# Kernel optimization log

Hardware: AMD Instinct MI355X
Metric: run time of the kernel (lower is better)

Reference implementation:

```python
import jax, jax.numpy as jnp
import numpy as np

N, E, D = 50000, 800000, 128
CLAMP = 2.0  # coord_weights_clamp_value


def setup_inputs() -> dict:
    key = jax.random.key(0)
    ks = jax.random.split(key, 12)
    rn = lambda k, shape, scale: jax.random.normal(k, shape, jnp.float32) * scale
    s = lambda fan_in: 1.0 / np.sqrt(fan_in)
    h = rn(ks[0], (N, D), 1.0)
    x = rn(ks[1], (N, 3), 1.0)
    edges = jax.random.randint(ks[2], (2, E), 0, N)
    # edge MLP: Linear(2D+1 -> D), SiLU, Linear(D -> D), SiLU
    we1 = rn(ks[3], (2 * D + 1, D), s(2 * D + 1)); be1 = jnp.zeros((D,), jnp.float32)
    we2 = rn(ks[4], (D, D), s(D));                 be2 = jnp.zeros((D,), jnp.float32)
    # node MLP: Linear(2D -> D), SiLU, Linear(D -> D)
    wn1 = rn(ks[5], (2 * D, D), s(2 * D));         bn1 = jnp.zeros((D,), jnp.float32)
    wn2 = rn(ks[6], (D, D), s(D));                 bn2 = jnp.zeros((D,), jnp.float32)
    # coord MLP: Linear(D -> D), SiLU, Linear(D -> 1, no bias, small init)
    wc1 = rn(ks[7], (D, D), s(D));                 bc1 = jnp.zeros((D,), jnp.float32)
    wc2 = rn(ks[8], (D, 1), 0.001)
    return dict(h=h, x=x, edges=edges, we1=we1, be1=be1, we2=we2, be2=be2,
                wn1=wn1, bn1=bn1, wn2=wn2, bn2=bn2, wc1=wc1, bc1=bc1, wc2=wc2)


def reference(h, x, edges, we1, be1, we2, be2, wn1, bn1, wn2, bn2, wc1, bc1, wc2):
    n = h.shape[0]
    row, col = edges[0], edges[1]
    # coord2radial
    coord_diff = x[row] - x[col]                                  # [E, 3]
    radial = jnp.sum(coord_diff * coord_diff, axis=1, keepdims=True)  # [E, 1]
    # edge model: phi_e(h_i, h_j, ||x_i - x_j||^2)
    e_in = jnp.concatenate([h[row], h[col], radial], axis=1)      # [E, 2D+1]
    m = jax.nn.silu(jax.nn.silu(e_in @ we1 + be1) @ we2 + be2)    # [E, D]
    # coord model: x_i += mean_j (x_i - x_j) * phi_x(m_ij), clamped
    w = jax.nn.silu(m @ wc1 + bc1) @ wc2                          # [E, 1]
    trans = jnp.clip(coord_diff * w, -CLAMP, CLAMP)               # [E, 3]
    ones = jnp.ones((row.shape[0], 1), m.dtype)
    cnt = jax.ops.segment_sum(ones, row, num_segments=n)          # [N, 1]
    agg_x = jax.ops.segment_sum(trans, row, num_segments=n) / jnp.maximum(cnt, 1.0)
    x_out = x + agg_x
    # node model: h_i += phi_h(h_i, sum_j m_ij)  (residual=True)
    agg_m = jax.ops.segment_sum(m, row, num_segments=n)           # [N, D]
    h_up = jax.nn.silu(jnp.concatenate([h, agg_m], axis=1) @ wn1 + bn1) @ wn2 + bn2
    h_out = h + h_up
    return (h_out, x_out)
```

## Files before the change

### kernel.cpp

```cpp
#include <hip/hip_runtime.h>
#include <hip/hip_bf16.h>
#include <stdint.h>

typedef unsigned short u16;
typedef __bf16 bf16x8 __attribute__((ext_vector_type(8)));
typedef float f32x4 __attribute__((ext_vector_type(4)));

#define DD 128

__device__ __forceinline__ u16 f2bf(float f) {
  uint32_t r;
  asm("v_cvt_pk_bf16_f32 %0, %1, %2" : "=v"(r) : "v"(f), "v"(f));
  return (u16)r;
}
__device__ __forceinline__ float bf2f(u16 h) {
  union { uint32_t u; float f; } v; v.u = ((uint32_t)h) << 16;
  return v.f;
}
__device__ __forceinline__ uint32_t pack2(float a, float b) {
  uint32_t r;
  asm("v_cvt_pk_bf16_f32 %0, %1, %2" : "=v"(r) : "v"(a), "v"(b));
  return r;
}
__device__ __forceinline__ float silu_(float v) {
  return v * __builtin_amdgcn_rcpf(1.0f + __expf(-v));
}
__device__ __forceinline__ f32x4 MFMA(bf16x8 a, bf16x8 b, f32x4 c) {
  return __builtin_amdgcn_mfma_f32_16x16x32_bf16(a, b, c, 0, 0, 0);
}
#define LGKM_FENCE() do { asm volatile("s_waitcnt lgkmcnt(0)" ::: "memory"); __builtin_amdgcn_sched_barrier(0); } while (0)

__global__ __launch_bounds__(256) void kprep(
    const float* __restrict__ we1, const float* __restrict__ we2,
    const float* __restrict__ wn1, const float* __restrict__ wn2,
    const float* __restrict__ wc1, u16* __restrict__ frags) {
  const int total = 16384 * 5 + 32768;
  for (int idx = blockIdx.x * blockDim.x + threadIdx.x; idx < total;
       idx += gridDim.x * blockDim.x) {
    const float* src; int segbase;
    if (idx < 16384)      { src = we1;          segbase = 0; }
    else if (idx < 32768) { src = we1 + 16384;  segbase = 16384; }
    else if (idx < 49152) { src = we2;          segbase = 32768; }
    else if (idx < 65536) { src = wc1;          segbase = 49152; }
    else if (idx < 81920) { src = wn2;          segbase = 65536; }
    else                  { src = wn1;          segbase = 81920; }
    int local = idx - segbase;
    int k = local >> 7, n = local & 127;
    float v = src[k * 128 + n];
    int s = k >> 5, i = k & 7, g = (k >> 3) & 3;
    int lane = (g << 4) | (n & 15), f = n >> 4;
    frags[segbase + (((s * 8 + f) * 64 + lane) << 3) + i] = f2bf(v);
  }
}

__global__ __launch_bounds__(256) void kpq(
    const float* __restrict__ h, const float* __restrict__ be1,
    const u16* __restrict__ wA, const u16* __restrict__ wB,
    u16* __restrict__ Pb, u16* __restrict__ Qb, int N) {
  __shared__ u16 act[64 * 128];
  const int tid = threadIdx.x;
  const int w = tid >> 6, l = tid & 63;
  const int lm = l & 15, lh = l >> 4;
  const int base = blockIdx.x * 64;

  {
    const int q = l & 3;
    const int rowL = w * 16 + (l >> 2);
    int node = base + rowL; if (node >= N) node = N - 1;
    const float* hs = h + (size_t)node * 128 + q * 32;
    #pragma unroll
    for (int c4 = 0; c4 < 4; ++c4) {
      float4 v0 = *(const float4*)(hs + c4 * 8);
      float4 v1 = *(const float4*)(hs + c4 * 8 + 4);
      uint4 pk;
      pk.x = pack2(v0.x, v0.y); pk.y = pack2(v0.z, v0.w);
      pk.z = pack2(v1.x, v1.y); pk.w = pack2(v1.z, v1.w);
      int c = q * 4 + c4;
      *(uint4*)&act[rowL * 128 + (((c ^ (rowL & 7))) << 3)] = pk;
    }
  }
  LGKM_FENCE();
  const int rowA = w * 16 + lm, sw = rowA & 7;
  bf16x8 a[4];
  #pragma unroll
  for (int s = 0; s < 4; ++s)
    a[s] = *(const bf16x8*)&act[rowA * 128 + (((4 * s + lh) ^ sw) << 3)];
  float be1r[8];
  #pragma unroll
  for (int f = 0; f < 8; ++f) be1r[f] = be1[16 * f + lm];

  f32x4 acc[8] = {};
  #pragma unroll
  for (int s = 0; s < 4; ++s)
    #pragma unroll
    for (int f = 0; f < 8; ++f)
      acc[f] = MFMA(a[s], *(const bf16x8*)(wA + (((s * 8 + f) * 64 + l) << 3)), acc[f]);
  #pragma unroll
  for (int f = 0; f < 8; ++f)
    #pragma unroll
    for (int r = 0; r < 4; ++r) {
      int row = base + w * 16 + lh * 4 + r;
      Pb[(size_t)row * 128 + 16 * f + lm] = f2bf(acc[f][r] + be1r[f]);
    }

  f32x4 acc2[8] = {};
  #pragma unroll
  for (int s = 0; s < 4; ++s)
    #pragma unroll
    for (int f = 0; f < 8; ++f)
      acc2[f] = MFMA(a[s], *(const bf16x8*)(wB + (((s * 8 + f) * 64 + l) << 3)), acc2[f]);
  #pragma unroll
  for (int f = 0; f < 8; ++f)
    #pragma unroll
    for (int r = 0; r < 4; ++r) {
      int row = base + w * 16 + lh * 4 + r;
      Qb[(size_t)row * 128 + 16 * f + lm] = f2bf(acc2[f][r]);
    }
}


__global__ __launch_bounds__(256) void kedgeA(
    const float* __restrict__ x, const int* __restrict__ edges,
    const float* __restrict__ we1, const float* __restrict__ be2,
    const float* __restrict__ bc1, const float* __restrict__ wc2,
    const u16* __restrict__ Pb, const u16* __restrict__ Qb,
    const u16* __restrict__ we2f, const u16* __restrict__ wc1f,
    u16* __restrict__ mT, float* __restrict__ trans4, int E) {
  __shared__ u16 act[64 * 128];
  __shared__ float w1c[128];
  const int tid = threadIdx.x;
  if (tid < 128) w1c[tid] = we1[256 * 128 + tid];
  __syncthreads();

  const int w = tid >> 6, l = tid & 63;
  const int lm = l & 15, lh = l >> 4;
  float be2r[8], bc1r[8], wc2r[8];
  #pragma unroll
  for (int f = 0; f < 8; ++f) {
    be2r[f] = be2[16 * f + lm];
    bc1r[f] = bc1[16 * f + lm];
    wc2r[f] = wc2[16 * f + lm];
  }

  const int tb = blockIdx.x * 64 + w * 16;
  int eMine = tb + lm;
  int eC = eMine < E ? eMine : E - 1;
  const int rowv = edges[eC];
  const int colv = edges[E + eC];
  float cdx = x[rowv * 3]     - x[colv * 3];
  float cdy = x[rowv * 3 + 1] - x[colv * 3 + 1];
  float cdz = x[rowv * 3 + 2] - x[colv * 3 + 2];
  float radial = cdx * cdx + cdy * cdy + cdz * cdz;

  {
    const int el = l >> 2, q = l & 3;
    int rG = __shfl(rowv, el), cG = __shfl(colv, el);
    float rad = __shfl(radial, el);
    const int rowL = w * 16 + el;
    const u16* Pp = Pb + (size_t)rG * 128 + q * 32;
    const u16* Qp = Qb + (size_t)cG * 128 + q * 32;
    #pragma unroll
    for (int c4 = 0; c4 < 4; ++c4) {
      uint4 pv = *(const uint4*)(Pp + c4 * 8);
      uint4 qv = *(const uint4*)(Qp + c4 * 8);
      uint32_t pw[4] = {pv.x, pv.y, pv.z, pv.w};
      uint32_t qw[4] = {qv.x, qv.y, qv.z, qv.w};
      uint32_t ow[4];
      #pragma unroll
      for (int jj = 0; jj < 4; ++jj) {
        int fb = q * 32 + c4 * 8 + jj * 2;
        float t0 = bf2f((u16)(pw[jj] & 0xffff)) + bf2f((u16)(qw[jj] & 0xffff)) + rad * w1c[fb];
        float t1 = bf2f((u16)(pw[jj] >> 16))    + bf2f((u16)(qw[jj] >> 16))    + rad * w1c[fb + 1];
        ow[jj] = pack2(silu_(t0), silu_(t1));
      }
      int c = q * 4 + c4;
      *(uint4*)&act[rowL * 128 + ((c ^ (rowL & 7)) << 3)] =
          make_uint4(ow[0], ow[1], ow[2], ow[3]);
    }
  }
  LGKM_FENCE();

  const int rowA = w * 16 + lm, sw = rowA & 7;
  bf16x8 a[4];
  #pragma unroll
  for (int s = 0; s < 4; ++s)
    a[s] = *(const bf16x8*)&act[rowA * 128 + (((4 * s + lh) ^ sw) << 3)];

  f32x4 acc[8] = {};
  #pragma unroll
  for (int s = 0; s < 4; ++s)
    #pragma unroll
    for (int f = 0; f < 8; ++f)
      acc[f] = MFMA(a[s], *(const bf16x8*)(we2f + (((s * 8 + f) * 64 + l) << 3)), acc[f]);

  bool ev[4];
  #pragma unroll
  for (int r = 0; r < 4; ++r) ev[r] = (tb + lh * 4 + r) < E;
  u16* mTb = mT + (size_t)(blockIdx.x * 4 + w) * 2048;

  #pragma unroll
  for (int f = 0; f < 8; ++f)
    #pragma unroll
    for (int r = 0; r < 4; ++r) {
      float m = silu_(acc[f][r] + be2r[f]);
      u16 mv = f2bf(m);
      int row = w * 16 + lh * 4 + r, col = 16 * f + lm;
      act[row * 128 + (((col >> 3) ^ (row & 7)) << 3) + (col & 7)] = mv;
      if (ev[r]) mTb[((lh * 4 + r) * 16 + lm) * 8 + f] = mv;
    }
  LGKM_FENCE();

  bf16x8 a2[4];
  #pragma unroll
  for (int s = 0; s < 4; ++s)
    a2[s] = *(const bf16x8*)&act[rowA * 128 + (((4 * s + lh) ^ sw) << 3)];
  f32x4 acc3[8] = {};
  #pragma unroll
  for (int s = 0; s < 4; ++s)
    #pragma unroll
    for (int f = 0; f < 8; ++f)
      acc3[f] = MFMA(a2[s], *(const bf16x8*)(wc1f + (((s * 8 + f) * 64 + l) << 3)), acc3[f]);

  float wp[4] = {0.f, 0.f, 0.f, 0.f};
  #pragma unroll
  for (int f = 0; f < 8; ++f)
    #pragma unroll
    for (int r = 0; r < 4; ++r)
      wp[r] += silu_(acc3[f][r] + bc1r[f]) * wc2r[f];
  #pragma unroll
  for (int r = 0; r < 4; ++r) {
    wp[r] += __shfl_xor(wp[r], 1);
    wp[r] += __shfl_xor(wp[r], 2);
    wp[r] += __shfl_xor(wp[r], 4);
    wp[r] += __shfl_xor(wp[r], 8);
  }
  #pragma unroll
  for (int r = 0; r < 4; ++r) {
    int erv = __shfl(rowv, lh * 4 + r);
    float cdxr = __shfl(cdx, lh * 4 + r);
    float cdyr = __shfl(cdy, lh * 4 + r);
    float cdzr = __shfl(cdz, lh * 4 + r);
    if (lm < 4 && ev[r]) {
      float wv = wp[r];
      float v3;
      if (lm == 0)      v3 = fminf(fmaxf(cdxr * wv, -2.0f), 2.0f);
      else if (lm == 1) v3 = fminf(fmaxf(cdyr * wv, -2.0f), 2.0f);
      else if (lm == 2) v3 = fminf(fmaxf(cdzr * wv, -2.0f), 2.0f);
      else              v3 = __int_as_float(erv);
      trans4[(size_t)(tb + lh * 4 + r) * 4 + lm] = v3;
    }
  }
}

__global__ __launch_bounds__(256) void kscat(
    const u16* __restrict__ mT, const float* __restrict__ trans4,
    float* __restrict__ aggm, float* __restrict__ aggx, int E) {
  const int tid = threadIdx.x;
  const int w = tid >> 6, l = tid & 63;
  const int lh = l >> 4, lm = l & 15;
  const int tile = blockIdx.x * 4 + w;
  const int tb = tile * 16;

  const u16* base = mT + (size_t)tile * 2048;
  bf16x8 ch[4];
  #pragma unroll
  for (int r = 0; r < 4; ++r)
    ch[r] = *(const bf16x8*)(base + ((lh * 4 + r) * 16 + lm) * 8);

  int eL = tb + (l >> 2);
  float tv = (eL < E) ? trans4[(size_t)eL * 4 + (l & 3)] : __int_as_float(-1);

  int erOwn = __float_as_int(__shfl(tv, (l >> 2) * 4 + 3));
  if (erOwn >= 0) {
    float val = ((l & 3) == 3) ? 1.0f : tv;
    unsafeAtomicAdd(&aggx[(size_t)erOwn * 4 + (l & 3)], val);
  }

  #pragma unroll
  for (int r = 0; r < 4; ++r) {
    int er = __float_as_int(__shfl(tv, (lh * 4 + r) * 4 + 3));
    if (er >= 0) {
      const u16* hp = (const u16*)&ch[r];
      #pragma unroll
      for (int f = 0; f < 8; ++f)
        unsafeAtomicAdd(&aggm[(size_t)er * 128 + 16 * f + lm], bf2f(hp[f]));
    }
  }
}

__global__ __launch_bounds__(256) void kedge_mono(
    const float* __restrict__ x, const int* __restrict__ edges,
    const float* __restrict__ we1, const float* __restrict__ be2,
    const float* __restrict__ bc1, const float* __restrict__ wc2,
    const u16* __restrict__ Pb, const u16* __restrict__ Qb,
    const u16* __restrict__ we2f, const u16* __restrict__ wc1f,
    float* __restrict__ aggm, float* __restrict__ aggx, int E) {
  __shared__ u16 act[64 * 128];
  __shared__ float w1c[128];
  const int tid = threadIdx.x;
  if (tid < 128) w1c[tid] = we1[256 * 128 + tid];
  __syncthreads();

  const int w = tid >> 6, l = tid & 63;
  const int lm = l & 15, lh = l >> 4;
  float be2r[8], bc1r[8], wc2r[8];
  #pragma unroll
  for (int f = 0; f < 8; ++f) {
    be2r[f] = be2[16 * f + lm];
    bc1r[f] = bc1[16 * f + lm];
    wc2r[f] = wc2[16 * f + lm];
  }

  const int tb = blockIdx.x * 64 + w * 16;
  int eMine = tb + lm;
  int eC = eMine < E ? eMine : E - 1;
  const int rowv = edges[eC];
  const int colv = edges[E + eC];
  float cdx = x[rowv * 3]     - x[colv * 3];
  float cdy = x[rowv * 3 + 1] - x[colv * 3 + 1];
  float cdz = x[rowv * 3 + 2] - x[colv * 3 + 2];
  float radial = cdx * cdx + cdy * cdy + cdz * cdz;

  {
    const int el = l >> 2, q = l & 3;
    int rG = __shfl(rowv, el), cG = __shfl(colv, el);
    float rad = __shfl(radial, el);
    const int rowL = w * 16 + el;
    const u16* Pp = Pb + (size_t)rG * 128 + q * 32;
    const u16* Qp = Qb + (size_t)cG * 128 + q * 32;
    #pragma unroll
    for (int c4 = 0; c4 < 4; ++c4) {
      uint4 pv = *(const uint4*)(Pp + c4 * 8);
      uint4 qv = *(const uint4*)(Qp + c4 * 8);
      uint32_t pw[4] = {pv.x, pv.y, pv.z, pv.w};
      uint32_t qw[4] = {qv.x, qv.y, qv.z, qv.w};
      uint32_t ow[4];
      #pragma unroll
      for (int jj = 0; jj < 4; ++jj) {
        int fb = q * 32 + c4 * 8 + jj * 2;
        float t0 = bf2f((u16)(pw[jj] & 0xffff)) + bf2f((u16)(qw[jj] & 0xffff)) + rad * w1c[fb];
        float t1 = bf2f((u16)(pw[jj] >> 16))    + bf2f((u16)(qw[jj] >> 16))    + rad * w1c[fb + 1];
        ow[jj] = pack2(silu_(t0), silu_(t1));
      }
      int c = q * 4 + c4;
      *(uint4*)&act[rowL * 128 + ((c ^ (rowL & 7)) << 3)] =
          make_uint4(ow[0], ow[1], ow[2], ow[3]);
    }
  }
  LGKM_FENCE();

  const int rowA = w * 16 + lm, sw = rowA & 7;
  bf16x8 a[4];
  #pragma unroll
  for (int s = 0; s < 4; ++s)
    a[s] = *(const bf16x8*)&act[rowA * 128 + (((4 * s + lh) ^ sw) << 3)];

  f32x4 acc[8] = {};
  #pragma unroll
  for (int s = 0; s < 4; ++s)
    #pragma unroll
    for (int f = 0; f < 8; ++f)
      acc[f] = MFMA(a[s], *(const bf16x8*)(we2f + (((s * 8 + f) * 64 + l) << 3)), acc[f]);

  #pragma unroll
  for (int f = 0; f < 8; ++f)
    #pragma unroll
    for (int r = 0; r < 4; ++r) {
      float m = silu_(acc[f][r] + be2r[f]);
      int row = w * 16 + lh * 4 + r, col = 16 * f + lm;
      act[row * 128 + (((col >> 3) ^ (row & 7)) << 3) + (col & 7)] = f2bf(m);
    }
  LGKM_FENCE();

  bf16x8 a2[4];
  #pragma unroll
  for (int s = 0; s < 4; ++s)
    a2[s] = *(const bf16x8*)&act[rowA * 128 + (((4 * s + lh) ^ sw) << 3)];
  f32x4 acc3[8] = {};
  #pragma unroll
  for (int s = 0; s < 4; ++s)
    #pragma unroll
    for (int f = 0; f < 8; ++f)
      acc3[f] = MFMA(a2[s], *(const bf16x8*)(wc1f + (((s * 8 + f) * 64 + l) << 3)), acc3[f]);

  float wp[4] = {0.f, 0.f, 0.f, 0.f};
  #pragma unroll
  for (int f = 0; f < 8; ++f)
    #pragma unroll
    for (int r = 0; r < 4; ++r)
      wp[r] += silu_(acc3[f][r] + bc1r[f]) * wc2r[f];
  #pragma unroll
  for (int r = 0; r < 4; ++r) {
    wp[r] += __shfl_xor(wp[r], 1);
    wp[r] += __shfl_xor(wp[r], 2);
    wp[r] += __shfl_xor(wp[r], 4);
    wp[r] += __shfl_xor(wp[r], 8);
  }
  int er[4]; bool vr[4];
  float cdxr[4], cdyr[4], cdzr[4];
  #pragma unroll
  for (int r = 0; r < 4; ++r) {
    er[r] = __shfl(rowv, lh * 4 + r);
    vr[r] = (tb + lh * 4 + r) < E;
    cdxr[r] = __shfl(cdx, lh * 4 + r);
    cdyr[r] = __shfl(cdy, lh * 4 + r);
    cdzr[r] = __shfl(cdz, lh * 4 + r);
  }

  if (lm < 4) {
    #pragma unroll
    for (int r = 0; r < 4; ++r) {
      if (vr[r]) {
        float wv = wp[r];
        float v3;
        if (lm == 0)      v3 = fminf(fmaxf(cdxr[r] * wv, -2.0f), 2.0f);
        else if (lm == 1) v3 = fminf(fmaxf(cdyr[r] * wv, -2.0f), 2.0f);
        else if (lm == 2) v3 = fminf(fmaxf(cdzr[r] * wv, -2.0f), 2.0f);
        else              v3 = 1.0f;
        unsafeAtomicAdd(&aggx[(size_t)er[r] * 4 + lm], v3);
      }
    }
  }
  #pragma unroll
  for (int f = 0; f < 8; ++f)
    #pragma unroll
    for (int r = 0; r < 4; ++r) {
      if (vr[r]) {
        float m = silu_(acc[f][r] + be2r[f]);
        unsafeAtomicAdd(&aggm[(size_t)er[r] * 128 + 16 * f + lm], m);
      }
    }
}

__global__ __launch_bounds__(256) void knode(
    const float* __restrict__ h, const float* __restrict__ x,
    const float* __restrict__ aggm, const float* __restrict__ aggx,
    const float* __restrict__ bn1, const float* __restrict__ bn2,
    const u16* __restrict__ wn1f, const u16* __restrict__ wn2f,
    float* __restrict__ out, int N) {
  __shared__ u16 act[64 * 256];
  __shared__ u16 act2[64 * 128];
  const int tid = threadIdx.x;
  const int w = tid >> 6, l = tid & 63;
  const int lm = l & 15, lh = l >> 4;
  const int base = blockIdx.x * 64;

  if (tid < 192) {
    int n = base + tid / 3, c = tid - (tid / 3) * 3;
    if (n < N) {
      float ct = fmaxf(aggx[(size_t)n * 4 + 3], 1.0f);
      out[(size_t)N * 128 + (size_t)n * 3 + c] =
          x[(size_t)n * 3 + c] + aggx[(size_t)n * 4 + c] / ct;
    }
  }

  {
    const int q = l & 3;
    const int rowL = w * 16 + (l >> 2);
    int node = base + rowL; if (node >= N) node = N - 1;
    const float* src = (q < 2) ? (h + (size_t)node * 128 + q * 64)
                               : (aggm + (size_t)node * 128 + (q - 2) * 64);
    #pragma unroll
    for (int c8 = 0; c8 < 8; ++c8) {
      float4 v0 = *(const float4*)(src + c8 * 8);
      float4 v1 = *(const float4*)(src + c8 * 8 + 4);
      uint4 pk;
      pk.x = pack2(v0.x, v0.y); pk.y = pack2(v0.z, v0.w);
      pk.z = pack2(v1.x, v1.y); pk.w = pack2(v1.z, v1.w);
      int c = q * 8 + c8;
      *(uint4*)&act[rowL * 256 + ((c ^ (rowL & 7)) << 3)] = pk;
    }
  }
  LGKM_FENCE();

  const int rowA = w * 16 + lm, sw = rowA & 7;
  float bn1r[8], bn2r[8];
  #pragma unroll
  for (int f = 0; f < 8; ++f) {
    bn1r[f] = bn1[16 * f + lm];
    bn2r[f] = bn2[16 * f + lm];
  }
  bf16x8 a[8];
  #pragma unroll
  for (int s = 0; s < 8; ++s)
    a[s] = *(const bf16x8*)&act[rowA * 256 + (((4 * s + lh) ^ sw) << 3)];
  f32x4 acc[8] = {};
  #pragma unroll
  for (int s = 0; s < 8; ++s)
    #pragma unroll
    for (int f = 0; f < 8; ++f)
      acc[f] = MFMA(a[s], *(const bf16x8*)(wn1f + (((s * 8 + f) * 64 + l) << 3)), acc[f]);
  #pragma unroll
  for (int f = 0; f < 8; ++f)
    #pragma unroll
    for (int r = 0; r < 4; ++r) {
      int row = w * 16 + lh * 4 + r, col = 16 * f + lm;
      act2[row * 128 + (((col >> 3) ^ (row & 7)) << 3) + (col & 7)] =
          f2bf(silu_(acc[f][r] + bn1r[f]));
    }
  LGKM_FENCE();

  bf16x8 a2[4];
  #pragma unroll
  for (int s = 0; s < 4; ++s)
    a2[s] = *(const bf16x8*)&act2[rowA * 128 + (((4 * s + lh) ^ sw) << 3)];
  f32x4 acc2[8] = {};
  #pragma unroll
  for (int s = 0; s < 4; ++s)
    #pragma unroll
    for (int f = 0; f < 8; ++f)
      acc2[f] = MFMA(a2[s], *(const bf16x8*)(wn2f + (((s * 8 + f) * 64 + l) << 3)), acc2[f]);
  #pragma unroll
  for (int f = 0; f < 8; ++f)
    #pragma unroll
    for (int r = 0; r < 4; ++r) {
      int n2 = base + w * 16 + lh * 4 + r;
      if (n2 < N) {
        int col = 16 * f + lm;
        out[(size_t)n2 * 128 + col] =
            h[(size_t)n2 * 128 + col] + acc2[f][r] + bn2r[f];
      }
    }
}

extern "C" void kernel_launch(void* const* d_in, const int* in_sizes, int n_in,
                              void* d_out, int out_size, void* d_ws, size_t ws_size,
                              hipStream_t stream) {
  const float* h   = (const float*)d_in[0];
  const float* x   = (const float*)d_in[1];
  const int* edges = (const int*)d_in[2];
  const float* we1 = (const float*)d_in[3];
  const float* be1 = (const float*)d_in[4];
  const float* we2 = (const float*)d_in[5];
  const float* be2 = (const float*)d_in[6];
  const float* wn1 = (const float*)d_in[7];
  const float* bn1 = (const float*)d_in[8];
  const float* wn2 = (const float*)d_in[9];
  const float* bn2 = (const float*)d_in[10];
  const float* wc1 = (const float*)d_in[11];
  const float* bc1 = (const float*)d_in[12];
  const float* wc2 = (const float*)d_in[13];

  const int N = in_sizes[0] / DD;
  const int E = in_sizes[2] / 2;
  const int NT = (N + 63) & ~63;
  const int ET = (E + 15) & ~15;

  u16* Pb    = (u16*)d_ws;
  u16* Qb    = Pb + (size_t)NT * DD;
  u16* frags = Qb + (size_t)NT * DD;
  float* aggm = (float*)(frags + 114688);
  float* aggx = aggm + (size_t)NT * DD;
  u16* mT     = (u16*)(aggx + (size_t)NT * 4);
  float* trans4 = (float*)(mT + (size_t)ET * DD);

  size_t need_small = (size_t)NT * DD * 2 * 2 + 114688 * 2 +
                      (size_t)NT * (DD * 4 + 16);
  size_t need_big = need_small + (size_t)ET * DD * 2 + (size_t)ET * 16;
  if (ws_size < need_small) return;

  hipMemsetAsync(aggm, 0, (size_t)NT * (DD * 4 + 16), stream);
  hipLaunchKernelGGL(kprep, dim3(64), dim3(256), 0, stream,
                     we1, we2, wn1, wn2, wc1, frags);
  hipLaunchKernelGGL(kpq, dim3(NT / 64), dim3(256), 0, stream,
                     h, be1, frags, frags + 16384, Pb, Qb, N);
  if (ws_size >= need_big) {
    hipLaunchKernelGGL(kedgeA, dim3((E + 63) / 64), dim3(256), 0, stream,
                       x, edges, we1, be2, bc1, wc2, Pb, Qb,
                       frags + 32768, frags + 49152, mT, trans4, E);
    hipLaunchKernelGGL(kscat, dim3((ET / 16 + 3) / 4), dim3(256), 0, stream,
                       mT, trans4, aggm, aggx, E);
  } else {
    hipLaunchKernelGGL(kedge_mono, dim3((E + 63) / 64), dim3(256), 0, stream,
                       x, edges, we1, be2, bc1, wc2, Pb, Qb,
                       frags + 32768, frags + 49152, aggm, aggx, E);
  }
  hipLaunchKernelGGL(knode, dim3(NT / 64), dim3(256), 0, stream,
                     h, x, aggm, aggx, bn1, bn2,
                     frags + 81920, frags + 65536, (float*)d_out, N);
}
```

Baseline: 453.9 us.

## Build CSR by destination row and aggregate edges per node without atomics

Adds count, scan and scatter kernels that group edge ids by destination row. A new per-node edge kernel gives each wavefront one node and walks its edges in tiles of 16. It accumulates the message sum and clamped coordinate translations in registers and writes aggm and x_out directly. This removes the intermediate message buffer writes and reads and the per-element float atomics of the scatter pass. In exchange it pays for CSR construction, including a single-block serial scan, and for wasted MFMA work on partially filled tiles when node degree is not a multiple of 16.

```diff
diff --git a/kernel.cpp b/kernel.cpp
--- a/kernel.cpp
+++ b/kernel.cpp
@@ -53,6 +53,48 @@
   }
 }
 
+__global__ __launch_bounds__(256) void kcount(
+    const int* __restrict__ edges, int* __restrict__ cnt2, int E) {
+  int i = blockIdx.x * blockDim.x + threadIdx.x;
+  if (i < E) atomicAdd(&cnt2[edges[i]], 1);
+}
+
+__global__ __launch_bounds__(256) void kscan(
+    int* __restrict__ cnt2, int* __restrict__ rowptr, int N, int E) {
+  __shared__ int part[256];
+  const int t = threadIdx.x;
+  const int C = (N + 255) / 256;
+  const int lo = t * C, hi = min(lo + C, N);
+  int s = 0;
+  for (int i = lo; i < hi; ++i) s += cnt2[i];
+  part[t] = s;
+  __syncthreads();
+  if (t == 0) {
+    int run = 0;
+    for (int i = 0; i < 256; ++i) { int v = part[i]; part[i] = run; run += v; }
+  }
+  __syncthreads();
+  int run = part[t];
+  for (int i = lo; i < hi; ++i) {
+    int v = cnt2[i];
+    rowptr[i] = run;
+    run += v;
+    cnt2[i] = 0;
+  }
+  if (t == 0) rowptr[N] = E;
+}
+
+__global__ __launch_bounds__(256) void kscatter(
+    const int* __restrict__ edges, const int* __restrict__ rowptr,
+    int* __restrict__ cnt2, int* __restrict__ eids, int E) {
+  int i = blockIdx.x * blockDim.x + threadIdx.x;
+  if (i < E) {
+    int r = edges[i];
+    int pos = rowptr[r] + atomicAdd(&cnt2[r], 1);
+    eids[pos] = i;
+  }
+}
+
 __global__ __launch_bounds__(256) void kpq(
     const float* __restrict__ h, const float* __restrict__ be1,
     const u16* __restrict__ wA, const u16* __restrict__ wB,
@@ -118,14 +160,175 @@
     }
 }
 
-
-__global__ __launch_bounds__(256) void kedgeA(
+__global__ __launch_bounds__(256) void kedgeC(
     const float* __restrict__ x, const int* __restrict__ edges,
     const float* __restrict__ we1, const float* __restrict__ be2,
     const float* __restrict__ bc1, const float* __restrict__ wc2,
     const u16* __restrict__ Pb, const u16* __restrict__ Qb,
     const u16* __restrict__ we2f, const u16* __restrict__ wc1f,
-    u16* __restrict__ mT, float* __restrict__ trans4, int E) {
+    const int* __restrict__ rowptr, const int* __restrict__ eids,
+    float* __restrict__ aggm, float* __restrict__ xout, int E, int N) {
+  __shared__ u16 act[64 * 128];
+  __shared__ float w1c[128];
+  const int tid = threadIdx.x;
+  if (tid < 128) w1c[tid] = we1[256 * 128 + tid];
+  __syncthreads();
+
+  const int w = tid >> 6, l = tid & 63;
+  const int lm = l & 15, lh = l >> 4;
+  const int n = blockIdx.x * 4 + w;
+  if (n >= N) return;
+
+  const int start = rowptr[n];
+  const int deg = rowptr[n + 1] - start;
+
+  float be2r[8], bc1r[8], wc2r[8];
+  #pragma unroll
+  for (int f = 0; f < 8; ++f) {
+    be2r[f] = be2[16 * f + lm];
+    bc1r[f] = bc1[16 * f + lm];
+    wc2r[f] = wc2[16 * f + lm];
+  }
+
+  const int q = l & 3, el = l >> 2;
+  uint4 pnv[4];
+  #pragma unroll
+  for (int c4 = 0; c4 < 4; ++c4)
+    pnv[c4] = *(const uint4*)(Pb + (size_t)n * 128 + q * 32 + c4 * 8);
+  const float xn0 = x[n * 3], xn1 = x[n * 3 + 1], xn2 = x[n * 3 + 2];
+
+  const int rowA = w * 16 + lm, sw = rowA & 7;
+  float aggr[8] = {};
+  float ax = 0.f, ay = 0.f, az = 0.f;
+  const int ntile = (deg + 15) >> 4;
+
+  for (int t = 0; t < ntile; ++t) {
+    const int myo = t * 16 + lm;
+    const int eid = eids[start + (myo < deg ? myo : 0)];
+    const int colv = edges[E + eid];
+    float cdx = xn0 - x[colv * 3];
+    float cdy = xn1 - x[colv * 3 + 1];
+    float cdz = xn2 - x[colv * 3 + 2];
+    float radial = cdx * cdx + cdy * cdy + cdz * cdz;
+
+    {
+      const int cG = __shfl(colv, el);
+      const float rad = __shfl(radial, el);
+      const int rowL = w * 16 + el;
+      const u16* Qp = Qb + (size_t)cG * 128 + q * 32;
+      #pragma unroll
+      for (int c4 = 0; c4 < 4; ++c4) {
+        uint4 qv = *(const uint4*)(Qp + c4 * 8);
+        uint32_t pw[4] = {pnv[c4].x, pnv[c4].y, pnv[c4].z, pnv[c4].w};
+        uint32_t qw[4] = {qv.x, qv.y, qv.z, qv.w};
+        uint32_t ow[4];
+        #pragma unroll
+        for (int jj = 0; jj < 4; ++jj) {
+          int fb = q * 32 + c4 * 8 + jj * 2;
+          float t0 = bf2f((u16)(pw[jj] & 0xffff)) + bf2f((u16)(qw[jj] & 0xffff)) + rad * w1c[fb];
+          float t1 = bf2f((u16)(pw[jj] >> 16))    + bf2f((u16)(qw[jj] >> 16))    + rad * w1c[fb + 1];
+          ow[jj] = pack2(silu_(t0), silu_(t1));
+        }
+        int c = q * 4 + c4;
+        *(uint4*)&act[rowL * 128 + ((c ^ (rowL & 7)) << 3)] =
+            make_uint4(ow[0], ow[1], ow[2], ow[3]);
+      }
+    }
+    LGKM_FENCE();
+
+    bf16x8 a[4];
+    #pragma unroll
+    for (int s = 0; s < 4; ++s)
+      a[s] = *(const bf16x8*)&act[rowA * 128 + (((4 * s + lh) ^ sw) << 3)];
+
+    f32x4 acc[8] = {};
+    #pragma unroll
+    for (int s = 0; s < 4; ++s)
+      #pragma unroll
+      for (int f = 0; f < 8; ++f)
+        acc[f] = MFMA(a[s], *(const bf16x8*)(we2f + (((s * 8 + f) * 64 + l) << 3)), acc[f]);
+
+    bool vr[4];
+    #pragma unroll
+    for (int r = 0; r < 4; ++r) vr[r] = (t * 16 + lh * 4 + r) < deg;
+
+    #pragma unroll
+    for (int f = 0; f < 8; ++f)
+      #pragma unroll
+      for (int r = 0; r < 4; ++r) {
+        float m = silu_(acc[f][r] + be2r[f]);
+        if (vr[r]) aggr[f] += m;
+        int row = w * 16 + lh * 4 + r, col = 16 * f + lm;
+        act[row * 128 + (((col >> 3) ^ (row & 7)) << 3) + (col & 7)] = f2bf(m);
+      }
+    LGKM_FENCE();
+
+    bf16x8 a2[4];
+    #pragma unroll
+    for (int s = 0; s < 4; ++s)
+      a2[s] = *(const bf16x8*)&act[rowA * 128 + (((4 * s + lh) ^ sw) << 3)];
+    f32x4 acc3[8] = {};
+    #pragma unroll
+    for (int s = 0; s < 4; ++s)
+      #pragma unroll
+      for (int f = 0; f < 8; ++f)
+        acc3[f] = MFMA(a2[s], *(const bf16x8*)(wc1f + (((s * 8 + f) * 64 + l) << 3)), acc3[f]);
+
+    float wp[4] = {0.f, 0.f, 0.f, 0.f};
+    #pragma unroll
+    for (int f = 0; f < 8; ++f)
+      #pragma unroll
+      for (int r = 0; r < 4; ++r)
+        wp[r] += silu_(acc3[f][r] + bc1r[f]) * wc2r[f];
+    #pragma unroll
+    for (int r = 0; r < 4; ++r) {
+      wp[r] += __shfl_xor(wp[r], 1);
+      wp[r] += __shfl_xor(wp[r], 2);
+      wp[r] += __shfl_xor(wp[r], 4);
+      wp[r] += __shfl_xor(wp[r], 8);
+    }
+    #pragma unroll
+    for (int r = 0; r < 4; ++r) {
+      float cdxr = __shfl(cdx, lh * 4 + r);
+      float cdyr = __shfl(cdy, lh * 4 + r);
+      float cdzr = __shfl(cdz, lh * 4 + r);
+      if (vr[r]) {
+        float wv = wp[r];
+        ax += fminf(fmaxf(cdxr * wv, -2.0f), 2.0f);
+        ay += fminf(fmaxf(cdyr * wv, -2.0f), 2.0f);
+        az += fminf(fmaxf(cdzr * wv, -2.0f), 2.0f);
+      }
+    }
+  }
+
+  #pragma unroll
+  for (int f = 0; f < 8; ++f) {
+    aggr[f] += __shfl_xor(aggr[f], 16);
+    aggr[f] += __shfl_xor(aggr[f], 32);
+  }
+  if (lh == 0) {
+    #pragma unroll
+    for (int f = 0; f < 8; ++f)
+      aggm[(size_t)n * 128 + 16 * f + lm] = aggr[f];
+  }
+  ax += __shfl_xor(ax, 16); ax += __shfl_xor(ax, 32);
+  ay += __shfl_xor(ay, 16); ay += __shfl_xor(ay, 32);
+  az += __shfl_xor(az, 16); az += __shfl_xor(az, 32);
+  if (l == 0) {
+    float dv = fmaxf((float)deg, 1.0f);
+    xout[(size_t)n * 3 + 0] = xn0 + ax / dv;
+    xout[(size_t)n * 3 + 1] = xn1 + ay / dv;
+    xout[(size_t)n * 3 + 2] = xn2 + az / dv;
+  }
+}
+
+__global__ __launch_bounds__(256) void kedge_mono(
+    const float* __restrict__ x, const int* __restrict__ edges,
+    const float* __restrict__ we1, const float* __restrict__ be2,
+    const float* __restrict__ bc1, const float* __restrict__ wc2,
+    const u16* __restrict__ Pb, const u16* __restrict__ Qb,
+    const u16* __restrict__ we2f, const u16* __restrict__ wc1f,
+    float* __restrict__ aggm, float* __restrict__ aggx, int E) {
   __shared__ u16 act[64 * 128];
   __shared__ float w1c[128];
   const int tid = threadIdx.x;
@@ -193,175 +396,6 @@
     for (int f = 0; f < 8; ++f)
       acc[f] = MFMA(a[s], *(const bf16x8*)(we2f + (((s * 8 + f) * 64 + l) << 3)), acc[f]);
 
-  bool ev[4];
-  #pragma unroll
-  for (int r = 0; r < 4; ++r) ev[r] = (tb + lh * 4 + r) < E;
-  u16* mTb = mT + (size_t)(blockIdx.x * 4 + w) * 2048;
-
-  #pragma unroll
-  for (int f = 0; f < 8; ++f)
-    #pragma unroll
-    for (int r = 0; r < 4; ++r) {
-      float m = silu_(acc[f][r] + be2r[f]);
-      u16 mv = f2bf(m);
-      int row = w * 16 + lh * 4 + r, col = 16 * f + lm;
-      act[row * 128 + (((col >> 3) ^ (row & 7)) << 3) + (col & 7)] = mv;
-      if (ev[r]) mTb[((lh * 4 + r) * 16 + lm) * 8 + f] = mv;
-    }
-  LGKM_FENCE();
-
-  bf16x8 a2[4];
-  #pragma unroll
-  for (int s = 0; s < 4; ++s)
-    a2[s] = *(const bf16x8*)&act[rowA * 128 + (((4 * s + lh) ^ sw) << 3)];
-  f32x4 acc3[8] = {};
-  #pragma unroll
-  for (int s = 0; s < 4; ++s)
-    #pragma unroll
-    for (int f = 0; f < 8; ++f)
-      acc3[f] = MFMA(a2[s], *(const bf16x8*)(wc1f + (((s * 8 + f) * 64 + l) << 3)), acc3[f]);
-
-  float wp[4] = {0.f, 0.f, 0.f, 0.f};
-  #pragma unroll
-  for (int f = 0; f < 8; ++f)
-    #pragma unroll
-    for (int r = 0; r < 4; ++r)
-      wp[r] += silu_(acc3[f][r] + bc1r[f]) * wc2r[f];
-  #pragma unroll
-  for (int r = 0; r < 4; ++r) {
-    wp[r] += __shfl_xor(wp[r], 1);
-    wp[r] += __shfl_xor(wp[r], 2);
-    wp[r] += __shfl_xor(wp[r], 4);
-    wp[r] += __shfl_xor(wp[r], 8);
-  }
-  #pragma unroll
-  for (int r = 0; r < 4; ++r) {
-    int erv = __shfl(rowv, lh * 4 + r);
-    float cdxr = __shfl(cdx, lh * 4 + r);
-    float cdyr = __shfl(cdy, lh * 4 + r);
-    float cdzr = __shfl(cdz, lh * 4 + r);
-    if (lm < 4 && ev[r]) {
-      float wv = wp[r];
-      float v3;
-      if (lm == 0)      v3 = fminf(fmaxf(cdxr * wv, -2.0f), 2.0f);
-      else if (lm == 1) v3 = fminf(fmaxf(cdyr * wv, -2.0f), 2.0f);
-      else if (lm == 2) v3 = fminf(fmaxf(cdzr * wv, -2.0f), 2.0f);
-      else              v3 = __int_as_float(erv);
-      trans4[(size_t)(tb + lh * 4 + r) * 4 + lm] = v3;
-    }
-  }
-}
-
-__global__ __launch_bounds__(256) void kscat(
-    const u16* __restrict__ mT, const float* __restrict__ trans4,
-    float* __restrict__ aggm, float* __restrict__ aggx, int E) {
-  const int tid = threadIdx.x;
-  const int w = tid >> 6, l = tid & 63;
-  const int lh = l >> 4, lm = l & 15;
-  const int tile = blockIdx.x * 4 + w;
-  const int tb = tile * 16;
-
-  const u16* base = mT + (size_t)tile * 2048;
-  bf16x8 ch[4];
-  #pragma unroll
-  for (int r = 0; r < 4; ++r)
-    ch[r] = *(const bf16x8*)(base + ((lh * 4 + r) * 16 + lm) * 8);
-
-  int eL = tb + (l >> 2);
-  float tv = (eL < E) ? trans4[(size_t)eL * 4 + (l & 3)] : __int_as_float(-1);
-
-  int erOwn = __float_as_int(__shfl(tv, (l >> 2) * 4 + 3));
-  if (erOwn >= 0) {
-    float val = ((l & 3) == 3) ? 1.0f : tv;
-    unsafeAtomicAdd(&aggx[(size_t)erOwn * 4 + (l & 3)], val);
-  }
-
-  #pragma unroll
-  for (int r = 0; r < 4; ++r) {
-    int er = __float_as_int(__shfl(tv, (lh * 4 + r) * 4 + 3));
-    if (er >= 0) {
-      const u16* hp = (const u16*)&ch[r];
-      #pragma unroll
-      for (int f = 0; f < 8; ++f)
-        unsafeAtomicAdd(&aggm[(size_t)er * 128 + 16 * f + lm], bf2f(hp[f]));
-    }
-  }
-}
-
-__global__ __launch_bounds__(256) void kedge_mono(
-    const float* __restrict__ x, const int* __restrict__ edges,
-    const float* __restrict__ we1, const float* __restrict__ be2,
-    const float* __restrict__ bc1, const float* __restrict__ wc2,
-    const u16* __restrict__ Pb, const u16* __restrict__ Qb,
-    const u16* __restrict__ we2f, const u16* __restrict__ wc1f,
-    float* __restrict__ aggm, float* __restrict__ aggx, int E) {
-  __shared__ u16 act[64 * 128];
-  __shared__ float w1c[128];
-  const int tid = threadIdx.x;
-  if (tid < 128) w1c[tid] = we1[256 * 128 + tid];
-  __syncthreads();
-
-  const int w = tid >> 6, l = tid & 63;
-  const int lm = l & 15, lh = l >> 4;
-  float be2r[8], bc1r[8], wc2r[8];
-  #pragma unroll
-  for (int f = 0; f < 8; ++f) {
-    be2r[f] = be2[16 * f + lm];
-    bc1r[f] = bc1[16 * f + lm];
-    wc2r[f] = wc2[16 * f + lm];
-  }
-
-  const int tb = blockIdx.x * 64 + w * 16;
-  int eMine = tb + lm;
-  int eC = eMine < E ? eMine : E - 1;
-  const int rowv = edges[eC];
-  const int colv = edges[E + eC];
-  float cdx = x[rowv * 3]     - x[colv * 3];
-  float cdy = x[rowv * 3 + 1] - x[colv * 3 + 1];
-  float cdz = x[rowv * 3 + 2] - x[colv * 3 + 2];
-  float radial = cdx * cdx + cdy * cdy + cdz * cdz;
-
-  {
-    const int el = l >> 2, q = l & 3;
-    int rG = __shfl(rowv, el), cG = __shfl(colv, el);
-    float rad = __shfl(radial, el);
-    const int rowL = w * 16 + el;
-    const u16* Pp = Pb + (size_t)rG * 128 + q * 32;
-    const u16* Qp = Qb + (size_t)cG * 128 + q * 32;
-    #pragma unroll
-    for (int c4 = 0; c4 < 4; ++c4) {
-      uint4 pv = *(const uint4*)(Pp + c4 * 8);
-      uint4 qv = *(const uint4*)(Qp + c4 * 8);
-      uint32_t pw[4] = {pv.x, pv.y, pv.z, pv.w};
-      uint32_t qw[4] = {qv.x, qv.y, qv.z, qv.w};
-      uint32_t ow[4];
-      #pragma unroll
-      for (int jj = 0; jj < 4; ++jj) {
-        int fb = q * 32 + c4 * 8 + jj * 2;
-        float t0 = bf2f((u16)(pw[jj] & 0xffff)) + bf2f((u16)(qw[jj] & 0xffff)) + rad * w1c[fb];
-        float t1 = bf2f((u16)(pw[jj] >> 16))    + bf2f((u16)(qw[jj] >> 16))    + rad * w1c[fb + 1];
-        ow[jj] = pack2(silu_(t0), silu_(t1));
-      }
-      int c = q * 4 + c4;
-      *(uint4*)&act[rowL * 128 + ((c ^ (rowL & 7)) << 3)] =
-          make_uint4(ow[0], ow[1], ow[2], ow[3]);
-    }
-  }
-  LGKM_FENCE();
-
-  const int rowA = w * 16 + lm, sw = rowA & 7;
-  bf16x8 a[4];
-  #pragma unroll
-  for (int s = 0; s < 4; ++s)
-    a[s] = *(const bf16x8*)&act[rowA * 128 + (((4 * s + lh) ^ sw) << 3)];
-
-  f32x4 acc[8] = {};
-  #pragma unroll
-  for (int s = 0; s < 4; ++s)
-    #pragma unroll
-    for (int f = 0; f < 8; ++f)
-      acc[f] = MFMA(a[s], *(const bf16x8*)(we2f + (((s * 8 + f) * 64 + l) << 3)), acc[f]);
-
   #pragma unroll
   for (int f = 0; f < 8; ++f)
     #pragma unroll
@@ -437,7 +471,7 @@
     const float* __restrict__ aggm, const float* __restrict__ aggx,
     const float* __restrict__ bn1, const float* __restrict__ bn2,
     const u16* __restrict__ wn1f, const u16* __restrict__ wn2f,
-    float* __restrict__ out, int N) {
+    float* __restrict__ out, int N, int do_x) {
   __shared__ u16 act[64 * 256];
   __shared__ u16 act2[64 * 128];
   const int tid = threadIdx.x;
@@ -445,7 +479,7 @@
   const int lm = l & 15, lh = l >> 4;
   const int base = blockIdx.x * 64;
 
-  if (tid < 192) {
+  if (do_x && tid < 192) {
     int n = base + tid / 3, c = tid - (tid / 3) * 3;
     if (n < N) {
       float ct = fmaxf(aggx[(size_t)n * 4 + 3], 1.0f);
@@ -544,38 +578,48 @@
   const int N = in_sizes[0] / DD;
   const int E = in_sizes[2] / 2;
   const int NT = (N + 63) & ~63;
-  const int ET = (E + 15) & ~15;
 
   u16* Pb    = (u16*)d_ws;
   u16* Qb    = Pb + (size_t)NT * DD;
   u16* frags = Qb + (size_t)NT * DD;
   float* aggm = (float*)(frags + 114688);
   float* aggx = aggm + (size_t)NT * DD;
-  u16* mT     = (u16*)(aggx + (size_t)NT * 4);
-  float* trans4 = (float*)(mT + (size_t)ET * DD);
-
-  size_t need_small = (size_t)NT * DD * 2 * 2 + 114688 * 2 +
-                      (size_t)NT * (DD * 4 + 16);
-  size_t need_big = need_small + (size_t)ET * DD * 2 + (size_t)ET * 16;
-  if (ws_size < need_small) return;
-
-  hipMemsetAsync(aggm, 0, (size_t)NT * (DD * 4 + 16), stream);
+  int* rowptr = (int*)(aggx + (size_t)NT * 4);
+  int* cnt2   = rowptr + (N + 1);
+  int* eids   = cnt2 + N;
+
+  size_t need_mono = (size_t)NT * DD * 2 * 2 + 114688 * 2 +
+                     (size_t)NT * (DD * 4 + 16);
+  size_t need_csr = need_mono + ((size_t)(N + 1) + N + E) * 4;
+  if (ws_size < need_mono) return;
+
   hipLaunchKernelGGL(kprep, dim3(64), dim3(256), 0, stream,
                      we1, we2, wn1, wn2, wc1, frags);
   hipLaunchKernelGGL(kpq, dim3(NT / 64), dim3(256), 0, stream,
                      h, be1, frags, frags + 16384, Pb, Qb, N);
-  if (ws_size >= need_big) {
-    hipLaunchKernelGGL(kedgeA, dim3((E + 63) / 64), dim3(256), 0, stream,
+
+  if (ws_size >= need_csr) {
+    hipMemsetAsync(cnt2, 0, (size_t)N * 4, stream);
+    hipLaunchKernelGGL(kcount, dim3((E + 255) / 256), dim3(256), 0, stream,
+                       edges, cnt2, E);
+    hipLaunchKernelGGL(kscan, dim3(1), dim3(256), 0, stream,
+                       cnt2, rowptr, N, E);
+    hipLaunchKernelGGL(kscatter, dim3((E + 255) / 256), dim3(256), 0, stream,
+                       edges, rowptr, cnt2, eids, E);
+    hipLaunchKernelGGL(kedgeC, dim3((N + 3) / 4), dim3(256), 0, stream,
                        x, edges, we1, be2, bc1, wc2, Pb, Qb,
-                       frags + 32768, frags + 49152, mT, trans4, E);
-    hipLaunchKernelGGL(kscat, dim3((ET / 16 + 3) / 4), dim3(256), 0, stream,
-                       mT, trans4, aggm, aggx, E);
+                       frags + 32768, frags + 49152, rowptr, eids,
+                       aggm, (float*)d_out + (size_t)N * 128, E, N);
+    hipLaunchKernelGGL(knode, dim3(NT / 64), dim3(256), 0, stream,
+                       h, x, aggm, aggx, bn1, bn2,
+                       frags + 81920, frags + 65536, (float*)d_out, N, 0);
   } else {
+    hipMemsetAsync(aggm, 0, (size_t)NT * (DD * 4 + 16), stream);
     hipLaunchKernelGGL(kedge_mono, dim3((E + 63) / 64), dim3(256), 0, stream,
                        x, edges, we1, be2, bc1, wc2, Pb, Qb,
                        frags + 32768, frags + 49152, aggm, aggx, E);
-  }
-  hipLaunchKernelGGL(knode, dim3(NT / 64), dim3(256), 0, stream,
-                     h, x, aggm, aggx, bn1, bn2,
-                     frags + 81920, frags + 65536, (float*)d_out, N);
-}
+    hipLaunchKernelGGL(knode, dim3(NT / 64), dim3(256), 0, stream,
+                       h, x, aggm, aggx, bn1, bn2,
+                       frags + 81920, frags + 65536, (float*)d_out, N, 1);
+  }
+}
```

After: 1.329 ms. 193% more time.

## Sort edges by source node (CSR) and fuse segment reduction into edge kernel

Applied to the files above, without the earlier changes.

Adds a counting sort of edges by row (count, three-pass scan, scatter into packed row/col words), then runs the edge MLP on the sorted order and atomically accumulates into aggm/aggx directly. When the four rows a lane holds share a node, it pre-sums them and issues one atomic. This replaces the separate mT/trans4 intermediate buffers and scatter kernel. It also remaps block IDs so consecutive work stays on one XCD and loads Q with nontemporal hints. In exchange it adds several small serial-ish scan kernels and edge atomics, and the 16-bit packing limits N to 65536.

```diff
diff --git a/kernel.cpp b/kernel.cpp
--- a/kernel.cpp
+++ b/kernel.cpp
@@ -5,6 +5,7 @@
 typedef unsigned short u16;
 typedef __bf16 bf16x8 __attribute__((ext_vector_type(8)));
 typedef float f32x4 __attribute__((ext_vector_type(4)));
+typedef unsigned int u32x4 __attribute__((ext_vector_type(4)));
 
 #define DD 128
 
@@ -53,6 +54,61 @@
   }
 }
 
+__global__ __launch_bounds__(256) void kcount(
+    const int* __restrict__ edges, int* __restrict__ cnt2, int E) {
+  int i = blockIdx.x * blockDim.x + threadIdx.x;
+  if (i < E) atomicAdd(&cnt2[edges[i]], 1);
+}
+
+__global__ __launch_bounds__(256) void kscanA(
+    const int* __restrict__ cnt2, int* __restrict__ tsum, int N) {
+  int g = blockIdx.x * 256 + threadIdx.x;
+  int C = (N + 16383) >> 14;
+  int lo = g * C, hi = min(lo + C, N);
+  int s = 0;
+  for (int i = lo; i < hi; ++i) s += cnt2[i];
+  tsum[g] = s;
+}
+
+__global__ __launch_bounds__(256) void kscanB(int* __restrict__ tsum) {
+  __shared__ int part[256];
+  int t = threadIdx.x;
+  int base = t * 64;
+  int s = 0;
+  for (int i = 0; i < 64; ++i) s += tsum[base + i];
+  part[t] = s;
+  __syncthreads();
+  if (t == 0) {
+    int run = 0;
+    for (int i = 0; i < 256; ++i) { int v = part[i]; part[i] = run; run += v; }
+  }
+  __syncthreads();
+  int run = part[t];
+  for (int i = 0; i < 64; ++i) { int v = tsum[base + i]; tsum[base + i] = run; run += v; }
+}
+
+__global__ __launch_bounds__(256) void kscanC(
+    int* __restrict__ cnt2, int* __restrict__ rowptr,
+    const int* __restrict__ tsum, int N, int E) {
+  int g = blockIdx.x * 256 + threadIdx.x;
+  int C = (N + 16383) >> 14;
+  int lo = g * C, hi = min(lo + C, N);
+  int run = tsum[g];
+  for (int i = lo; i < hi; ++i) { rowptr[i] = run; run += cnt2[i]; cnt2[i] = 0; }
+  if (g == 0) rowptr[N] = E;
+}
+
+__global__ __launch_bounds__(256) void kscatter2(
+    const int* __restrict__ edges, const int* __restrict__ rowptr,
+    int* __restrict__ cnt2, unsigned* __restrict__ spack, int E) {
+  int i = blockIdx.x * blockDim.x + threadIdx.x;
+  if (i < E) {
+    int r = edges[i];
+    int pos = rowptr[r] + atomicAdd(&cnt2[r], 1);
+    spack[pos] = ((unsigned)r << 16) | (unsigned)edges[E + i];
+  }
+}
+
 __global__ __launch_bounds__(256) void kpq(
     const float* __restrict__ h, const float* __restrict__ be1,
     const u16* __restrict__ wA, const u16* __restrict__ wB,
@@ -118,14 +174,13 @@
     }
 }
 
-
-__global__ __launch_bounds__(256) void kedgeA(
-    const float* __restrict__ x, const int* __restrict__ edges,
+__global__ __launch_bounds__(256) void kedgeS(
+    const float* __restrict__ x, const unsigned* __restrict__ spack,
     const float* __restrict__ we1, const float* __restrict__ be2,
     const float* __restrict__ bc1, const float* __restrict__ wc2,
     const u16* __restrict__ Pb, const u16* __restrict__ Qb,
     const u16* __restrict__ we2f, const u16* __restrict__ wc1f,
-    u16* __restrict__ mT, float* __restrict__ trans4, int E) {
+    float* __restrict__ aggm, float* __restrict__ aggx, int E) {
   __shared__ u16 act[64 * 128];
   __shared__ float w1c[128];
   const int tid = threadIdx.x;
@@ -142,11 +197,18 @@
     wc2r[f] = wc2[16 * f + lm];
   }
 
-  const int tb = blockIdx.x * 64 + w * 16;
+  const int nb = gridDim.x;
+  const int orig = blockIdx.x;
+  const int xcd = orig & 7, jj0 = orig >> 3;
+  const int qb = nb >> 3, rb = nb & 7;
+  const int wgid = (xcd < rb ? xcd * (qb + 1) : rb * (qb + 1) + (xcd - rb) * qb) + jj0;
+
+  const int tb = wgid * 64 + w * 16;
   int eMine = tb + lm;
   int eC = eMine < E ? eMine : E - 1;
-  const int rowv = edges[eC];
-  const int colv = edges[E + eC];
+  const unsigned pk = spack[eC];
+  const int rowv = (int)(pk >> 16);
+  const int colv = (int)(pk & 0xffffu);
   float cdx = x[rowv * 3]     - x[colv * 3];
   float cdy = x[rowv * 3 + 1] - x[colv * 3 + 1];
   float cdz = x[rowv * 3 + 2] - x[colv * 3 + 2];
@@ -161,17 +223,17 @@
     const u16* Qp = Qb + (size_t)cG * 128 + q * 32;
     #pragma unroll
     for (int c4 = 0; c4 < 4; ++c4) {
-      uint4 pv = *(const uint4*)(Pp + c4 * 8);
-      uint4 qv = *(const uint4*)(Qp + c4 * 8);
+      u32x4 pv = *(const u32x4*)(Pp + c4 * 8);
+      u32x4 qv = __builtin_nontemporal_load((const u32x4*)(Qp + c4 * 8));
       uint32_t pw[4] = {pv.x, pv.y, pv.z, pv.w};
       uint32_t qw[4] = {qv.x, qv.y, qv.z, qv.w};
       uint32_t ow[4];
       #pragma unroll
-      for (int jj = 0; jj < 4; ++jj) {
-        int fb = q * 32 + c4 * 8 + jj * 2;
-        float t0 = bf2f((u16)(pw[jj] & 0xffff)) + bf2f((u16)(qw[jj] & 0xffff)) + rad * w1c[fb];
-        float t1 = bf2f((u16)(pw[jj] >> 16))    + bf2f((u16)(qw[jj] >> 16))    + rad * w1c[fb + 1];
-        ow[jj] = pack2(silu_(t0), silu_(t1));
+      for (int t2 = 0; t2 < 4; ++t2) {
+        int fb = q * 32 + c4 * 8 + t2 * 2;
+        float t0 = bf2f((u16)(pw[t2] & 0xffff)) + bf2f((u16)(qw[t2] & 0xffff)) + rad * w1c[fb];
+        float t1 = bf2f((u16)(pw[t2] >> 16))    + bf2f((u16)(qw[t2] >> 16))    + rad * w1c[fb + 1];
+        ow[t2] = pack2(silu_(t0), silu_(t1));
       }
       int c = q * 4 + c4;
       *(uint4*)&act[rowL * 128 + ((c ^ (rowL & 7)) << 3)] =
@@ -193,20 +255,13 @@
     for (int f = 0; f < 8; ++f)
       acc[f] = MFMA(a[s], *(const bf16x8*)(we2f + (((s * 8 + f) * 64 + l) << 3)), acc[f]);
 
-  bool ev[4];
-  #pragma unroll
-  for (int r = 0; r < 4; ++r) ev[r] = (tb + lh * 4 + r) < E;
-  u16* mTb = mT + (size_t)(blockIdx.x * 4 + w) * 2048;
-
   #pragma unroll
   for (int f = 0; f < 8; ++f)
     #pragma unroll
     for (int r = 0; r < 4; ++r) {
       float m = silu_(acc[f][r] + be2r[f]);
-      u16 mv = f2bf(m);
       int row = w * 16 + lh * 4 + r, col = 16 * f + lm;
-      act[row * 128 + (((col >> 3) ^ (row & 7)) << 3) + (col & 7)] = mv;
-      if (ev[r]) mTb[((lh * 4 + r) * 16 + lm) * 8 + f] = mv;
+      act[row * 128 + (((col >> 3) ^ (row & 7)) << 3) + (col & 7)] = f2bf(m);
     }
   LGKM_FENCE();
 
@@ -234,57 +289,69 @@
     wp[r] += __shfl_xor(wp[r], 4);
     wp[r] += __shfl_xor(wp[r], 8);
   }
+  int er[4]; bool vr[4];
+  float cdxr[4], cdyr[4], cdzr[4];
   #pragma unroll
   for (int r = 0; r < 4; ++r) {
-    int erv = __shfl(rowv, lh * 4 + r);
-    float cdxr = __shfl(cdx, lh * 4 + r);
-    float cdyr = __shfl(cdy, lh * 4 + r);
-    float cdzr = __shfl(cdz, lh * 4 + r);
-    if (lm < 4 && ev[r]) {
-      float wv = wp[r];
-      float v3;
-      if (lm == 0)      v3 = fminf(fmaxf(cdxr * wv, -2.0f), 2.0f);
-      else if (lm == 1) v3 = fminf(fmaxf(cdyr * wv, -2.0f), 2.0f);
-      else if (lm == 2) v3 = fminf(fmaxf(cdzr * wv, -2.0f), 2.0f);
-      else              v3 = __int_as_float(erv);
-      trans4[(size_t)(tb + lh * 4 + r) * 4 + lm] = v3;
-    }
-  }
-}
-
-__global__ __launch_bounds__(256) void kscat(
-    const u16* __restrict__ mT, const float* __restrict__ trans4,
-    float* __restrict__ aggm, float* __restrict__ aggx, int E) {
-  const int tid = threadIdx.x;
-  const int w = tid >> 6, l = tid & 63;
-  const int lh = l >> 4, lm = l & 15;
-  const int tile = blockIdx.x * 4 + w;
-  const int tb = tile * 16;
-
-  const u16* base = mT + (size_t)tile * 2048;
-  bf16x8 ch[4];
-  #pragma unroll
-  for (int r = 0; r < 4; ++r)
-    ch[r] = *(const bf16x8*)(base + ((lh * 4 + r) * 16 + lm) * 8);
-
-  int eL = tb + (l >> 2);
-  float tv = (eL < E) ? trans4[(size_t)eL * 4 + (l & 3)] : __int_as_float(-1);
-
-  int erOwn = __float_as_int(__shfl(tv, (l >> 2) * 4 + 3));
-  if (erOwn >= 0) {
-    float val = ((l & 3) == 3) ? 1.0f : tv;
-    unsafeAtomicAdd(&aggx[(size_t)erOwn * 4 + (l & 3)], val);
-  }
-
-  #pragma unroll
-  for (int r = 0; r < 4; ++r) {
-    int er = __float_as_int(__shfl(tv, (lh * 4 + r) * 4 + 3));
-    if (er >= 0) {
-      const u16* hp = (const u16*)&ch[r];
+    er[r] = __shfl(rowv, lh * 4 + r);
+    vr[r] = (tb + lh * 4 + r) < E;
+    cdxr[r] = __shfl(cdx, lh * 4 + r);
+    cdyr[r] = __shfl(cdy, lh * 4 + r);
+    cdzr[r] = __shfl(cdz, lh * 4 + r);
+  }
+  const bool same = (er[0] == er[1]) && (er[1] == er[2]) && (er[2] == er[3]);
+
+  if (lm < 4) {
+    if (same) {
+      float v3s = 0.f;
       #pragma unroll
-      for (int f = 0; f < 8; ++f)
-        unsafeAtomicAdd(&aggm[(size_t)er * 128 + 16 * f + lm], bf2f(hp[f]));
-    }
+      for (int r = 0; r < 4; ++r) {
+        if (vr[r]) {
+          float wv = wp[r];
+          if (lm == 0)      v3s += fminf(fmaxf(cdxr[r] * wv, -2.0f), 2.0f);
+          else if (lm == 1) v3s += fminf(fmaxf(cdyr[r] * wv, -2.0f), 2.0f);
+          else if (lm == 2) v3s += fminf(fmaxf(cdzr[r] * wv, -2.0f), 2.0f);
+          else              v3s += 1.0f;
+        }
+      }
+      if (vr[0]) unsafeAtomicAdd(&aggx[(size_t)er[0] * 4 + lm], v3s);
+    } else {
+      #pragma unroll
+      for (int r = 0; r < 4; ++r) {
+        if (vr[r]) {
+          float wv = wp[r];
+          float v3;
+          if (lm == 0)      v3 = fminf(fmaxf(cdxr[r] * wv, -2.0f), 2.0f);
+          else if (lm == 1) v3 = fminf(fmaxf(cdyr[r] * wv, -2.0f), 2.0f);
+          else if (lm == 2) v3 = fminf(fmaxf(cdzr[r] * wv, -2.0f), 2.0f);
+          else              v3 = 1.0f;
+          unsafeAtomicAdd(&aggx[(size_t)er[r] * 4 + lm], v3);
+        }
+      }
+    }
+  }
+
+  if (same) {
+    if (vr[0]) {
+      #pragma unroll
+      for (int f = 0; f < 8; ++f) {
+        float s = 0.f;
+        #pragma unroll
+        for (int r = 0; r < 4; ++r)
+          if (vr[r]) s += silu_(acc[f][r] + be2r[f]);
+        unsafeAtomicAdd(&aggm[(size_t)er[0] * 128 + 16 * f + lm], s);
+      }
+    }
+  } else {
+    #pragma unroll
+    for (int f = 0; f < 8; ++f)
+      #pragma unroll
+      for (int r = 0; r < 4; ++r) {
+        if (vr[r]) {
+          float m = silu_(acc[f][r] + be2r[f]);
+          unsafeAtomicAdd(&aggm[(size_t)er[r] * 128 + 16 * f + lm], m);
+        }
+      }
   }
 }
 
@@ -336,11 +403,11 @@
       uint32_t qw[4] = {qv.x, qv.y, qv.z, qv.w};
       uint32_t ow[4];
       #pragma unroll
-      for (int jj = 0; jj < 4; ++jj) {
-        int fb = q * 32 + c4 * 8 + jj * 2;
-        float t0 = bf2f((u16)(pw[jj] & 0xffff)) + bf2f((u16)(qw[jj] & 0xffff)) + rad * w1c[fb];
-        float t1 = bf2f((u16)(pw[jj] >> 16))    + bf2f((u16)(qw[jj] >> 16))    + rad * w1c[fb + 1];
-        ow[jj] = pack2(silu_(t0), silu_(t1));
+      for (int t2 = 0; t2 < 4; ++t2) {
+        int fb = q * 32 + c4 * 8 + t2 * 2;
+        float t0 = bf2f((u16)(pw[t2] & 0xffff)) + bf2f((u16)(qw[t2] & 0xffff)) + rad * w1c[fb];
+        float t1 = bf2f((u16)(pw[t2] >> 16))    + bf2f((u16)(qw[t2] >> 16))    + rad * w1c[fb + 1];
+        ow[t2] = pack2(silu_(t0), silu_(t1));
       }
       int c = q * 4 + c4;
       *(uint4*)&act[rowL * 128 + ((c ^ (rowL & 7)) << 3)] =
@@ -544,32 +611,41 @@
   const int N = in_sizes[0] / DD;
   const int E = in_sizes[2] / 2;
   const int NT = (N + 63) & ~63;
-  const int ET = (E + 15) & ~15;
 
   u16* Pb    = (u16*)d_ws;
   u16* Qb    = Pb + (size_t)NT * DD;
   u16* frags = Qb + (size_t)NT * DD;
   float* aggm = (float*)(frags + 114688);
   float* aggx = aggm + (size_t)NT * DD;
-  u16* mT     = (u16*)(aggx + (size_t)NT * 4);
-  float* trans4 = (float*)(mT + (size_t)ET * DD);
-
-  size_t need_small = (size_t)NT * DD * 2 * 2 + 114688 * 2 +
-                      (size_t)NT * (DD * 4 + 16);
-  size_t need_big = need_small + (size_t)ET * DD * 2 + (size_t)ET * 16;
-  if (ws_size < need_small) return;
-
-  hipMemsetAsync(aggm, 0, (size_t)NT * (DD * 4 + 16), stream);
+  int* rowptr = (int*)(aggx + (size_t)NT * 4);
+  int* cnt2   = rowptr + (N + 1);
+  unsigned* spack = (unsigned*)(cnt2 + N);
+  int* tsum   = (int*)(spack + E);
+
+  size_t need_mono = (size_t)NT * DD * 2 * 2 + 114688 * 2 +
+                     (size_t)NT * (DD * 4 + 16);
+  size_t need_sort = need_mono + ((size_t)(N + 1) + N + E + 16384) * 4;
+  if (ws_size < need_mono) return;
+
   hipLaunchKernelGGL(kprep, dim3(64), dim3(256), 0, stream,
                      we1, we2, wn1, wn2, wc1, frags);
   hipLaunchKernelGGL(kpq, dim3(NT / 64), dim3(256), 0, stream,
                      h, be1, frags, frags + 16384, Pb, Qb, N);
-  if (ws_size >= need_big) {
-    hipLaunchKernelGGL(kedgeA, dim3((E + 63) / 64), dim3(256), 0, stream,
-                       x, edges, we1, be2, bc1, wc2, Pb, Qb,
-                       frags + 32768, frags + 49152, mT, trans4, E);
-    hipLaunchKernelGGL(kscat, dim3((ET / 16 + 3) / 4), dim3(256), 0, stream,
-                       mT, trans4, aggm, aggx, E);
+  hipMemsetAsync(aggm, 0, (size_t)NT * (DD * 4 + 16), stream);
+
+  if (ws_size >= need_sort && N <= 65536) {
+    hipMemsetAsync(cnt2, 0, (size_t)N * 4, stream);
+    hipLaunchKernelGGL(kcount, dim3((E + 255) / 256), dim3(256), 0, stream,
+                       edges, cnt2, E);
+    hipLaunchKernelGGL(kscanA, dim3(64), dim3(256), 0, stream, cnt2, tsum, N);
+    hipLaunchKernelGGL(kscanB, dim3(1), dim3(256), 0, stream, tsum);
+    hipLaunchKernelGGL(kscanC, dim3(64), dim3(256), 0, stream,
+                       cnt2, rowptr, tsum, N, E);
+    hipLaunchKernelGGL(kscatter2, dim3((E + 255) / 256), dim3(256), 0, stream,
+                       edges, rowptr, cnt2, spack, E);
+    hipLaunchKernelGGL(kedgeS, dim3((E + 63) / 64), dim3(256), 0, stream,
+                       x, spack, we1, be2, bc1, wc2, Pb, Qb,
+                       frags + 32768, frags + 49152, aggm, aggx, E);
   } else {
     hipLaunchKernelGGL(kedge_mono, dim3((E + 63) / 64), dim3(256), 0, stream,
                        x, edges, we1, be2, bc1, wc2, Pb, Qb,
```

New measurement: 522.5 us. 1.15x slower.
